# Kernel tuning notes

Hardware: AMD Instinct MI355X
Metric: run time of the kernel (lower is better)

## Reference

```python
import jax, jax.numpy as jnp
import numpy as np

N_NODES = 100000
N_EDGES = 800000
IN_FEATS = 128
OUT_FEATS = 128


def setup_inputs() -> dict:
    key = jax.random.key(0)
    k1, k2, k3, k4, k5, k6 = jax.random.split(key, 6)
    feat = jax.random.normal(k1, (N_NODES, IN_FEATS), dtype=jnp.float32)
    src = jax.random.randint(k2, (N_EDGES,), 0, N_NODES, dtype=jnp.int64)
    dst = jax.random.randint(k3, (N_EDGES,), 0, N_NODES, dtype=jnp.int64)
    # xavier_uniform with gain = calculate_gain('relu') = sqrt(2)
    gain = np.sqrt(2.0)
    lim = gain * np.sqrt(6.0 / (IN_FEATS + OUT_FEATS))
    W_neigh = jax.random.uniform(k4, (OUT_FEATS, IN_FEATS), minval=-lim, maxval=lim, dtype=jnp.float32)
    W_self = jax.random.uniform(k5, (OUT_FEATS, IN_FEATS), minval=-lim, maxval=lim, dtype=jnp.float32)
    b_lim = 1.0 / np.sqrt(IN_FEATS)
    b_self = jax.random.uniform(k6, (OUT_FEATS,), minval=-b_lim, maxval=b_lim, dtype=jnp.float32)
    return {"feat": feat, "src": src, "dst": dst, "W_neigh": W_neigh, "W_self": W_self, "b_self": b_self}


def reference(feat, src, dst, W_neigh, W_self, b_self):
    # copy_u + mean: gather source features along edges, segment-mean onto dst.
    # lin_before_mp is False (in_feats == out_feats), so aggregate raw features first.
    msgs = feat[src]                                   # [E, in_feats]
    summed = jax.ops.segment_sum(msgs, dst, num_segments=N_NODES)   # [N, in_feats]
    deg = jax.ops.segment_sum(jnp.ones((src.shape[0],), feat.dtype), dst, num_segments=N_NODES)
    h_neigh = summed / jnp.maximum(deg, 1.0)[:, None]  # mean; 0 for isolated nodes
    h_neigh = h_neigh @ W_neigh.T                      # fc_neigh (no bias)
    rst = feat @ W_self.T + b_self + h_neigh           # fc_self (bias) + neigh
    return rst
```

## Files before the change

### kernel.cpp

```cpp
#include <hip/hip_runtime.h>

#define N_NODES 100000
#define N_EDGES 800000
#define F 128
#define NB 16
#define BM 64

typedef __attribute__((ext_vector_type(8))) short bf16x8;
typedef __attribute__((ext_vector_type(4))) float f32x4;


__global__ void hist_kernel(const int* __restrict__ dst, int* __restrict__ count, int E) {
    int e = blockIdx.x * 256 + threadIdx.x;
    if (e < E) atomicAdd(&count[dst[e]], 1);
}

__global__ void scan1_kernel(const int* __restrict__ count, int* __restrict__ rowptr,
                             int* __restrict__ bsums, int N) {
    __shared__ int s[256];
    int tid = threadIdx.x;
    int base = blockIdx.x * 1024 + tid * 4;
    int c[4];
    int tsum = 0;
#pragma unroll
    for (int j = 0; j < 4; ++j) {
        int idx = base + j;
        c[j] = (idx < N) ? count[idx] : 0;
        tsum += c[j];
    }
    s[tid] = tsum;
    __syncthreads();
    for (int off = 1; off < 256; off <<= 1) {
        int u = (tid >= off) ? s[tid - off] : 0;
        __syncthreads();
        s[tid] += u;
        __syncthreads();
    }
    int incl = s[tid];
    int run = incl - tsum;
#pragma unroll
    for (int j = 0; j < 4; ++j) {
        int idx = base + j;
        if (idx < N) rowptr[idx] = run;
        run += c[j];
    }
    if (tid == 255) bsums[blockIdx.x] = incl;
}

__global__ void scan2_kernel(int* __restrict__ bsums, int nb) {
    __shared__ int s[256];
    int tid = threadIdx.x;
    int v = (tid < nb) ? bsums[tid] : 0;
    s[tid] = v;
    __syncthreads();
    for (int off = 1; off < 256; off <<= 1) {
        int u = (tid >= off) ? s[tid - off] : 0;
        __syncthreads();
        s[tid] += u;
        __syncthreads();
    }
    int excl = s[tid] - v;
    if (tid < nb) bsums[tid] = excl;
}

__global__ void scan3_kernel(int* __restrict__ rowptr, const int* __restrict__ bsums,
                             int* __restrict__ cursor, int N) {
    int i = blockIdx.x * 256 + threadIdx.x;
    if (i < N) {
        int r = rowptr[i] + bsums[i >> 10];
        rowptr[i] = r;
        cursor[i] = r;
    }
}

__global__ void fill_kernel(const int* __restrict__ src, const int* __restrict__ dst,
                            int* __restrict__ cursor, int* __restrict__ csr, int E) {
    int e = blockIdx.x * 256 + threadIdx.x;
    if (e < E) {
        int n = dst[e];
        int p = atomicAdd(&cursor[n], 1);
        csr[p] = src[e];
    }
}


__global__ void wprep_kernel(const float* __restrict__ Ws, const float* __restrict__ Wn,
                             short* __restrict__ wf) {
    int t = blockIdx.x * 256 + threadIdx.x;
    if (t >= 1024) return;
    int n = t >> 2;
    int ks = t & 3;
    const float* row = (n < 128) ? (Ws + (size_t)n * F) : (Wn + (size_t)(n - 128) * F);
    int ntile = n >> 4;
#pragma unroll
    for (int g = 0; g < 4; ++g) {
        int lane = (n & 15) + 16 * g;
        size_t base = ((size_t)(ntile * 4 + ks) * 64 + lane) * 8;
#pragma unroll
        for (int e = 0; e < 8; ++e) {
            float x = row[ks * 32 + g * 8 + e];
            unsigned xb = __float_as_uint(x);
            unsigned hb = xb & 0xFFFF0000u;
            float lo = x - __uint_as_float(hb);
            wf[base + e] = (short)(hb >> 16);
            wf[32768 + base + e] = (short)(__float_as_uint(lo) >> 16);
        }
    }
}


__global__ __launch_bounds__(256, 3) void gemm_mfma_kernel(
        const float* __restrict__ feat,
        const short* __restrict__ wf,
        const float* __restrict__ b_self,
        float* __restrict__ out, float* __restrict__ Y) {
    __shared__ bf16x8 aF[2][16][64];

    const int tid = threadIdx.x;
    const int nb = blockIdx.x * BM;

    {
        const int r = tid >> 2;
        const int ks = tid & 3;
        int n = nb + r;
        if (n >= N_NODES) n = N_NODES - 1;
        float4 v[8];
        const float4* g = reinterpret_cast<const float4*>(feat + (size_t)n * F + ks * 32);
#pragma unroll
        for (int j = 0; j < 8; ++j) v[j] = g[j];
        const float* vv = &v[0].x;
        const int mt = r >> 4;
        const int l0 = r & 15;
#pragma unroll
        for (int g5 = 0; g5 < 4; ++g5) {
            bf16x8 hi8, lo8;
#pragma unroll
            for (int e = 0; e < 8; ++e) {
                float x = vv[g5 * 8 + e];
                unsigned xb = __float_as_uint(x);
                unsigned hb = xb & 0xFFFF0000u;
                float lo = x - __uint_as_float(hb);
                hi8[e] = (short)(hb >> 16);
                lo8[e] = (short)(__float_as_uint(lo) >> 16);
            }
            aF[0][(ks << 2) | mt][l0 + 16 * g5] = hi8;
            aF[1][(ks << 2) | mt][l0 + 16 * g5] = lo8;
        }
    }
    __syncthreads();

    const int wv = tid >> 6;
    const int lane = tid & 63;

    f32x4 acc[4][4];
#pragma unroll
    for (int t = 0; t < 4; ++t)
#pragma unroll
        for (int j = 0; j < 4; ++j)
            acc[t][j] = (f32x4){0.f, 0.f, 0.f, 0.f};

    const bf16x8* wfh = reinterpret_cast<const bf16x8*>(wf);
    const bf16x8* wfl = wfh + 4096;

#pragma unroll
    for (int ks = 0; ks < 4; ++ks) {
        bf16x8 ah[4], al[4], bh[4], bl[4];
#pragma unroll
        for (int t = 0; t < 4; ++t) {
            ah[t] = aF[0][(ks << 2) | t][lane];
            al[t] = aF[1][(ks << 2) | t][lane];
        }
#pragma unroll
        for (int j = 0; j < 4; ++j) {
            const int ntile = wv * 4 + j;
            bh[j] = wfh[(ntile * 4 + ks) * 64 + lane];
            bl[j] = wfl[(ntile * 4 + ks) * 64 + lane];
        }
#pragma unroll
        for (int t = 0; t < 4; ++t)
#pragma unroll
            for (int j = 0; j < 4; ++j) {
                acc[t][j] = __builtin_amdgcn_mfma_f32_16x16x32_bf16(ah[t], bh[j], acc[t][j], 0, 0, 0);
                acc[t][j] = __builtin_amdgcn_mfma_f32_16x16x32_bf16(ah[t], bl[j], acc[t][j], 0, 0, 0);
                acc[t][j] = __builtin_amdgcn_mfma_f32_16x16x32_bf16(al[t], bh[j], acc[t][j], 0, 0, 0);
            }
    }

    const bool isOut = (wv < 2);
#pragma unroll
    for (int t = 0; t < 4; ++t) {
        const int m0 = nb + t * 16 + ((lane >> 4) << 2);
#pragma unroll
        for (int j = 0; j < 4; ++j) {
            const int col = wv * 64 + j * 16 + (lane & 15);
            if (isOut) {
                const float b = b_self[col];
#pragma unroll
                for (int r = 0; r < 4; ++r) {
                    const int m = m0 + r;
                    if (m < N_NODES) out[(size_t)m * F + col] = acc[t][j][r] + b;
                }
            } else {
#pragma unroll
                for (int r = 0; r < 4; ++r) {
                    const int m = m0 + r;
                    if (m < N_NODES) Y[(size_t)m * F + (col - 128)] = acc[t][j][r];
                }
            }
        }
    }
}


__global__ __launch_bounds__(256) void agg_kernel(
        const float* __restrict__ Y,
        const int* __restrict__ csr, const int* __restrict__ rowptr,
        const int* __restrict__ count,
        float* __restrict__ out) {
    const int node = blockIdx.x * 4 + (threadIdx.x >> 6);
    const int lane = threadIdx.x & 63;
    if (node >= N_NODES) return;

    const int rp = __builtin_amdgcn_readfirstlane(rowptr[node]);
    const int cnt = __builtin_amdgcn_readfirstlane(count[node]);

    float a0x = 0.f, a0y = 0.f, a1x = 0.f, a1y = 0.f;
    float a2x = 0.f, a2y = 0.f, a3x = 0.f, a3y = 0.f;

    int j = 0;
    for (; j + 4 <= cnt; j += 4) {
        const int i0 = csr[rp + j];
        const int i1 = csr[rp + j + 1];
        const int i2 = csr[rp + j + 2];
        const int i3 = csr[rp + j + 3];
        const float2 v0 = *reinterpret_cast<const float2*>(Y + (size_t)i0 * F + lane * 2);
        const float2 v1 = *reinterpret_cast<const float2*>(Y + (size_t)i1 * F + lane * 2);
        const float2 v2 = *reinterpret_cast<const float2*>(Y + (size_t)i2 * F + lane * 2);
        const float2 v3 = *reinterpret_cast<const float2*>(Y + (size_t)i3 * F + lane * 2);
        a0x += v0.x; a0y += v0.y;
        a1x += v1.x; a1y += v1.y;
        a2x += v2.x; a2y += v2.y;
        a3x += v3.x; a3y += v3.y;
    }
    for (; j < cnt; ++j) {
        const int i0 = csr[rp + j];
        const float2 v0 = *reinterpret_cast<const float2*>(Y + (size_t)i0 * F + lane * 2);
        a0x += v0.x; a0y += v0.y;
    }

    const float inv = 1.0f / fmaxf((float)cnt, 1.0f);
    const float sx = (a0x + a1x) + (a2x + a3x);
    const float sy = (a0y + a1y) + (a2y + a3y);

    float2* op = reinterpret_cast<float2*>(out + (size_t)node * F) + lane;
    float2 cur = *op;
    cur.x += sx * inv;
    cur.y += sy * inv;
    *op = cur;
}


__global__ __launch_bounds__(256) void main_kernel(
        const float* __restrict__ feat,
        const int* __restrict__ csr, const int* __restrict__ rowptr,
        const int* __restrict__ count,
        const float* __restrict__ Wn, const float* __restrict__ Ws,
        const float* __restrict__ b_self,
        float* __restrict__ out) {
    __shared__ __align__(16) float shF[NB][F];
    __shared__ __align__(16) float shH[NB][F];
    __shared__ __align__(16) float wts[32][F];
    __shared__ __align__(16) float wtn[32][F];

    const int tid = threadIdx.x;
    const int nb = blockIdx.x * NB;

    {
        const int g = tid >> 5;
        const int l = tid & 31;
        for (int i = g; i < NB; i += 8) {
            const int n = nb + i;
            const int rp = rowptr[n];
            const int cnt = count[n];
            float ax = 0.f, ay = 0.f, az = 0.f, aw = 0.f;
            for (int j = 0; j < cnt; ++j) {
                const int s = csr[rp + j];
                const float4 v = *reinterpret_cast<const float4*>(feat + (size_t)s * F + l * 4);
                ax += v.x; ay += v.y; az += v.z; aw += v.w;
            }
            const float dv = fmaxf((float)cnt, 1.0f);
            float4 h;
            h.x = ax / dv; h.y = ay / dv; h.z = az / dv; h.w = aw / dv;
            const float4 fv = *reinterpret_cast<const float4*>(feat + (size_t)n * F + l * 4);
            reinterpret_cast<float4*>(&shF[i][0])[l] = fv;
            reinterpret_cast<float4*>(&shH[i][0])[l] = h;
        }
    }
    __syncthreads();

    const int oc = tid & 63;
    const int ng = tid >> 6;
    float acc[4][2];
#pragma unroll
    for (int i = 0; i < 4; ++i) { acc[i][0] = 0.f; acc[i][1] = 0.f; }

    for (int kc = 0; kc < 4; ++kc) {
        {
            const int o_l = tid >> 1;
            const int k0 = (tid & 1) * 16;
            const float* gs = Ws + o_l * F + kc * 32 + k0;
            const float* gn = Wn + o_l * F + kc * 32 + k0;
#pragma unroll
            for (int j = 0; j < 16; ++j) {
                wts[k0 + j][o_l] = gs[j];
                wtn[k0 + j][o_l] = gn[j];
            }
        }
        __syncthreads();

#pragma unroll
        for (int kk4 = 0; kk4 < 32; kk4 += 4) {
            float4 fA[4], hA[4];
#pragma unroll
            for (int i = 0; i < 4; ++i) {
                const int node = ng * 4 + i;
                fA[i] = reinterpret_cast<const float4*>(&shF[node][0])[(kc * 32 + kk4) >> 2];
                hA[i] = reinterpret_cast<const float4*>(&shH[node][0])[(kc * 32 + kk4) >> 2];
            }
#pragma unroll
            for (int j = 0; j < 4; ++j) {
                const float2 wsv = *reinterpret_cast<const float2*>(&wts[kk4 + j][oc * 2]);
                const float2 wnv = *reinterpret_cast<const float2*>(&wtn[kk4 + j][oc * 2]);
#pragma unroll
                for (int i = 0; i < 4; ++i) {
                    const float fa = (&fA[i].x)[j];
                    const float ha = (&hA[i].x)[j];
                    acc[i][0] += fa * wsv.x + ha * wnv.x;
                    acc[i][1] += fa * wsv.y + ha * wnv.y;
                }
            }
        }
        __syncthreads();
    }

    const float b0 = b_self[oc * 2];
    const float b1 = b_self[oc * 2 + 1];
#pragma unroll
    for (int i = 0; i < 4; ++i) {
        const int n = nb + ng * 4 + i;
        float2 o2;
        o2.x = acc[i][0] + b0;
        o2.y = acc[i][1] + b1;
        *reinterpret_cast<float2*>(out + (size_t)n * F + oc * 2) = o2;
    }
}


extern "C" void kernel_launch(void* const* d_in, const int* in_sizes, int n_in,
                              void* d_out, int out_size, void* d_ws, size_t ws_size,
                              hipStream_t stream) {
    const float* feat = (const float*)d_in[0];
    const int* src    = (const int*)d_in[1];
    const int* dst    = (const int*)d_in[2];
    const float* Wn   = (const float*)d_in[3];
    const float* Ws   = (const float*)d_in[4];
    const float* bs   = (const float*)d_in[5];
    float* out        = (float*)d_out;

    const size_t y_floats = (size_t)N_NODES * F;
    const size_t wf_shorts = 65536;
    const size_t int_words = (size_t)3 * N_NODES + N_EDGES + 256;
    const size_t need = y_floats * 4 + wf_shorts * 2 + int_words * 4;
    const int nb1 = (N_NODES + 1023) / 1024;

    if (ws_size >= need) {
        float* Y    = (float*)d_ws;
        short* wf   = (short*)(Y + y_floats);
        int* count  = (int*)(wf + wf_shorts);
        int* rowptr = count + N_NODES;
        int* cursor = rowptr + N_NODES;
        int* csr    = cursor + N_NODES;
        int* bsums  = csr + N_EDGES;

        wprep_kernel<<<4, 256, 0, stream>>>(Ws, Wn, wf);
        hipMemsetAsync(count, 0, N_NODES * sizeof(int), stream);
        hist_kernel<<<(N_EDGES + 255) / 256, 256, 0, stream>>>(dst, count, N_EDGES);
        scan1_kernel<<<nb1, 256, 0, stream>>>(count, rowptr, bsums, N_NODES);
        scan2_kernel<<<1, 256, 0, stream>>>(bsums, nb1);
        scan3_kernel<<<(N_NODES + 255) / 256, 256, 0, stream>>>(rowptr, bsums, cursor, N_NODES);
        fill_kernel<<<(N_EDGES + 255) / 256, 256, 0, stream>>>(src, dst, cursor, csr, N_EDGES);
        gemm_mfma_kernel<<<(N_NODES + BM - 1) / BM, 256, 0, stream>>>(feat, wf, bs, out, Y);
        agg_kernel<<<(N_NODES + 3) / 4, 256, 0, stream>>>(Y, csr, rowptr, count, out);
    } else {
        int* count  = (int*)d_ws;
        int* rowptr = count + N_NODES;
        int* cursor = rowptr + N_NODES;
        int* csr    = cursor + N_NODES;
        int* bsums  = csr + N_EDGES;

        hipMemsetAsync(count, 0, N_NODES * sizeof(int), stream);
        hist_kernel<<<(N_EDGES + 255) / 256, 256, 0, stream>>>(dst, count, N_EDGES);
        scan1_kernel<<<nb1, 256, 0, stream>>>(count, rowptr, bsums, N_NODES);
        scan2_kernel<<<1, 256, 0, stream>>>(bsums, nb1);
        scan3_kernel<<<(N_NODES + 255) / 256, 256, 0, stream>>>(rowptr, bsums, cursor, N_NODES);
        fill_kernel<<<(N_EDGES + 255) / 256, 256, 0, stream>>>(src, dst, cursor, csr, N_EDGES);
        main_kernel<<<N_NODES / NB, 256, 0, stream>>>(feat, csr, rowptr, count, Wn, Ws, bs, out);
    }
}
```

Baseline: 288.7 us.

## Aggregate bf16 features before a fused dual GEMM, with a cooperative CSR build

```diff
diff --git a/kernel.cpp b/kernel.cpp
--- a/kernel.cpp
+++ b/kernel.cpp
@@ -1,13 +1,293 @@
 #include <hip/hip_runtime.h>
+#include <hip/hip_cooperative_groups.h>
+
+namespace cg = cooperative_groups;
 
 #define N_NODES 100000
 #define N_EDGES 800000
 #define F 128
 #define NB 16
 #define BM 64
+#define GBLK 512
+#define CS 196
 
 typedef __attribute__((ext_vector_type(8))) short bf16x8;
 typedef __attribute__((ext_vector_type(4))) float f32x4;
+
+__device__ inline unsigned short f2bf_rne(float x) {
+    unsigned u = __float_as_uint(x);
+    u += 0x7FFF + ((u >> 16) & 1);
+    return (unsigned short)(u >> 16);
+}
+
+
+__global__ void build_kernel(const int* __restrict__ src, const int* __restrict__ dst,
+                             const float* __restrict__ feat,
+                             const float* __restrict__ Ws, const float* __restrict__ Wn,
+                             unsigned* __restrict__ featbf, short* __restrict__ wf,
+                             int* __restrict__ count, int* __restrict__ rowptr,
+                             int* __restrict__ cursor, int* __restrict__ csr,
+                             int* __restrict__ bsums) {
+    cg::grid_group grid = cg::this_grid();
+    __shared__ int sh[256];
+    const int tid = threadIdx.x;
+    const int gt = blockIdx.x * 256 + tid;
+    const int GT = GBLK * 256;
+
+    for (int i = gt; i < N_NODES; i += GT) count[i] = 0;
+    {
+        const int total = N_NODES * (F / 8);
+        for (int i = gt; i < total; i += GT) {
+            const float4 a = reinterpret_cast<const float4*>(feat)[i * 2];
+            const float4 b = reinterpret_cast<const float4*>(feat)[i * 2 + 1];
+            uint4 r;
+            r.x = (unsigned)f2bf_rne(a.x) | ((unsigned)f2bf_rne(a.y) << 16);
+            r.y = (unsigned)f2bf_rne(a.z) | ((unsigned)f2bf_rne(a.w) << 16);
+            r.z = (unsigned)f2bf_rne(b.x) | ((unsigned)f2bf_rne(b.y) << 16);
+            r.w = (unsigned)f2bf_rne(b.z) | ((unsigned)f2bf_rne(b.w) << 16);
+            reinterpret_cast<uint4*>(featbf)[i] = r;
+        }
+    }
+    if (gt < 1024) {
+        const int n = gt >> 2;
+        const int ks = gt & 3;
+        const float* row;
+        short *hb_, *lb_;
+        int ntile;
+        if (n < 128) { row = Ws + (size_t)n * F; hb_ = wf;          lb_ = wf + 16384; ntile = n >> 4; }
+        else         { row = Wn + (size_t)(n - 128) * F; hb_ = wf + 32768; lb_ = wf + 49152; ntile = (n - 128) >> 4; }
+#pragma unroll
+        for (int g = 0; g < 4; ++g) {
+            const int lane = (n & 15) + 16 * g;
+            const size_t base = ((size_t)(ntile * 4 + ks) * 64 + lane) * 8;
+#pragma unroll
+            for (int e = 0; e < 8; ++e) {
+                const float x = row[ks * 32 + g * 8 + e];
+                const unsigned hb = __float_as_uint(x) & 0xFFFF0000u;
+                const float lo = x - __uint_as_float(hb);
+                hb_[base + e] = (short)(hb >> 16);
+                lb_[base + e] = (short)(__float_as_uint(lo) >> 16);
+            }
+        }
+    }
+    grid.sync();
+
+    for (int e = gt; e < N_EDGES; e += GT) atomicAdd(&count[dst[e]], 1);
+    grid.sync();
+
+    {
+        const int idx = blockIdx.x * CS + tid;
+        const int c = (tid < CS && idx < N_NODES) ? count[idx] : 0;
+        sh[tid] = c;
+        __syncthreads();
+        for (int off = 128; off > 0; off >>= 1) {
+            if (tid < off) sh[tid] += sh[tid + off];
+            __syncthreads();
+        }
+        if (tid == 0) bsums[blockIdx.x] = sh[0];
+    }
+    grid.sync();
+
+    if (blockIdx.x == 0) {
+        int carry = 0;
+        for (int r = 0; r < GBLK / 256; ++r) {
+            const int i = r * 256 + tid;
+            const int v = bsums[i];
+            sh[tid] = v;
+            __syncthreads();
+            for (int off = 1; off < 256; off <<= 1) {
+                const int u = (tid >= off) ? sh[tid - off] : 0;
+                __syncthreads();
+                sh[tid] += u;
+                __syncthreads();
+            }
+            bsums[i] = sh[tid] - v + carry;
+            carry += sh[255];
+            __syncthreads();
+        }
+    }
+    grid.sync();
+
+    {
+        const int idx = blockIdx.x * CS + tid;
+        const int c = (tid < CS && idx < N_NODES) ? count[idx] : 0;
+        sh[tid] = c;
+        __syncthreads();
+        for (int off = 1; off < 256; off <<= 1) {
+            const int u = (tid >= off) ? sh[tid - off] : 0;
+            __syncthreads();
+            sh[tid] += u;
+            __syncthreads();
+        }
+        if (tid < CS && idx < N_NODES) {
+            const int excl = bsums[blockIdx.x] + sh[tid] - c;
+            rowptr[idx] = excl;
+            cursor[idx] = excl;
+        }
+    }
+    grid.sync();
+
+    for (int e = gt; e < N_EDGES; e += GT) {
+        const int n = dst[e];
+        const int p = atomicAdd(&cursor[n], 1);
+        csr[p] = src[e];
+    }
+}
+
+
+__global__ __launch_bounds__(256) void agg_kernel(
+        const unsigned* __restrict__ featbf,
+        const int* __restrict__ csr, const int* __restrict__ rowptr,
+        const int* __restrict__ count,
+        unsigned* __restrict__ M) {
+    const int node = blockIdx.x * 4 + (threadIdx.x >> 6);
+    const int lane = threadIdx.x & 63;
+    if (node >= N_NODES) return;
+
+    const int rp = __builtin_amdgcn_readfirstlane(rowptr[node]);
+    const int cnt = __builtin_amdgcn_readfirstlane(count[node]);
+
+    float ax[8], ay[8];
+#pragma unroll
+    for (int u = 0; u < 8; ++u) { ax[u] = 0.f; ay[u] = 0.f; }
+
+    int j = 0;
+    for (; j + 8 <= cnt; j += 8) {
+        int idx[8];
+#pragma unroll
+        for (int u = 0; u < 8; ++u) idx[u] = __builtin_nontemporal_load(&csr[rp + j + u]);
+        unsigned v[8];
+#pragma unroll
+        for (int u = 0; u < 8; ++u) v[u] = featbf[(size_t)idx[u] * 64 + lane];
+#pragma unroll
+        for (int u = 0; u < 8; ++u) {
+            ax[u] += __uint_as_float(v[u] << 16);
+            ay[u] += __uint_as_float(v[u] & 0xFFFF0000u);
+        }
+    }
+    for (; j < cnt; ++j) {
+        const int i0 = __builtin_nontemporal_load(&csr[rp + j]);
+        const unsigned v = featbf[(size_t)i0 * 64 + lane];
+        ax[0] += __uint_as_float(v << 16);
+        ay[0] += __uint_as_float(v & 0xFFFF0000u);
+    }
+
+    const float inv = 1.0f / fmaxf((float)cnt, 1.0f);
+    float sx = 0.f, sy = 0.f;
+#pragma unroll
+    for (int u = 0; u < 8; ++u) { sx += ax[u]; sy += ay[u]; }
+    sx *= inv; sy *= inv;
+
+    const unsigned packed = (unsigned)f2bf_rne(sx) | ((unsigned)f2bf_rne(sy) << 16);
+    M[(size_t)node * 64 + lane] = packed;
+}
+
+
+__global__ __launch_bounds__(256, 3) void gemm_kernel(
+        const float* __restrict__ feat,
+        const unsigned* __restrict__ M,
+        const short* __restrict__ wf,
+        const float* __restrict__ b_self,
+        float* __restrict__ out) {
+    __shared__ bf16x8 aF[2][16][64];
+
+    const int tid = threadIdx.x;
+    const int nb = blockIdx.x * BM;
+
+    {
+        const int r = tid >> 2;
+        const int ks = tid & 3;
+        int n = nb + r;
+        if (n >= N_NODES) n = N_NODES - 1;
+        float4 v[8];
+        const float4* g = reinterpret_cast<const float4*>(feat + (size_t)n * F + ks * 32);
+#pragma unroll
+        for (int j = 0; j < 8; ++j) v[j] = g[j];
+        const float* vv = &v[0].x;
+        const int mt = r >> 4;
+        const int l0 = r & 15;
+#pragma unroll
+        for (int g5 = 0; g5 < 4; ++g5) {
+            bf16x8 hi8, lo8;
+#pragma unroll
+            for (int e = 0; e < 8; ++e) {
+                const float x = vv[g5 * 8 + e];
+                const unsigned hb = __float_as_uint(x) & 0xFFFF0000u;
+                const float lo = x - __uint_as_float(hb);
+                hi8[e] = (short)(hb >> 16);
+                lo8[e] = (short)(__float_as_uint(lo) >> 16);
+            }
+            aF[0][(ks << 2) | mt][l0 + 16 * g5] = hi8;
+            aF[1][(ks << 2) | mt][l0 + 16 * g5] = lo8;
+        }
+    }
+    __syncthreads();
+
+    const int wv = tid >> 6;
+    const int lane = tid & 63;
+
+    f32x4 acc[4][2];
+#pragma unroll
+    for (int t = 0; t < 4; ++t)
+#pragma unroll
+        for (int j = 0; j < 2; ++j)
+            acc[t][j] = (f32x4){0.f, 0.f, 0.f, 0.f};
+
+    const bf16x8* wsh = reinterpret_cast<const bf16x8*>(wf);
+    const bf16x8* wsl = wsh + 2048;
+    const bf16x8* wnh = wsh + 4096;
+    const bf16x8* wnl = wsh + 6144;
+    const bf16x8* M8 = reinterpret_cast<const bf16x8*>(M);
+
+#pragma unroll
+    for (int ks = 0; ks < 4; ++ks) {
+        bf16x8 ah[4], al[4], am[4];
+#pragma unroll
+        for (int t = 0; t < 4; ++t) {
+            ah[t] = aF[0][(ks << 2) | t][lane];
+            al[t] = aF[1][(ks << 2) | t][lane];
+        }
+#pragma unroll
+        for (int t = 0; t < 4; ++t) {
+            int node = nb + t * 16 + (lane & 15);
+            if (node >= N_NODES) node = N_NODES - 1;
+            am[t] = M8[(size_t)node * 16 + ks * 4 + (lane >> 4)];
+        }
+        bf16x8 bsh[2], bsl[2], bnh[2], bnl[2];
+#pragma unroll
+        for (int j = 0; j < 2; ++j) {
+            const int fi = ((wv * 2 + j) * 4 + ks) * 64 + lane;
+            bsh[j] = wsh[fi]; bsl[j] = wsl[fi];
+            bnh[j] = wnh[fi]; bnl[j] = wnl[fi];
+        }
+#pragma unroll
+        for (int t = 0; t < 4; ++t)
+#pragma unroll
+            for (int j = 0; j < 2; ++j) {
+                acc[t][j] = __builtin_amdgcn_mfma_f32_16x16x32_bf16(ah[t], bsh[j], acc[t][j], 0, 0, 0);
+                acc[t][j] = __builtin_amdgcn_mfma_f32_16x16x32_bf16(ah[t], bsl[j], acc[t][j], 0, 0, 0);
+                acc[t][j] = __builtin_amdgcn_mfma_f32_16x16x32_bf16(al[t], bsh[j], acc[t][j], 0, 0, 0);
+                acc[t][j] = __builtin_amdgcn_mfma_f32_16x16x32_bf16(am[t], bnh[j], acc[t][j], 0, 0, 0);
+                acc[t][j] = __builtin_amdgcn_mfma_f32_16x16x32_bf16(am[t], bnl[j], acc[t][j], 0, 0, 0);
+            }
+    }
+
+#pragma unroll
+    for (int t = 0; t < 4; ++t) {
+        const int m0 = nb + t * 16 + ((lane >> 4) << 2);
+#pragma unroll
+        for (int j = 0; j < 2; ++j) {
+            const int col = wv * 32 + j * 16 + (lane & 15);
+            const float b = b_self[col];
+#pragma unroll
+            for (int r = 0; r < 4; ++r) {
+                const int m = m0 + r;
+                if (m < N_NODES)
+                    __builtin_nontemporal_store(acc[t][j][r] + b, &out[(size_t)m * F + col]);
+            }
+        }
+    }
+}
 
 
 __global__ void hist_kernel(const int* __restrict__ dst, int* __restrict__ count, int E) {
@@ -82,183 +362,6 @@
         csr[p] = src[e];
     }
 }
-
-
-__global__ void wprep_kernel(const float* __restrict__ Ws, const float* __restrict__ Wn,
-                             short* __restrict__ wf) {
-    int t = blockIdx.x * 256 + threadIdx.x;
-    if (t >= 1024) return;
-    int n = t >> 2;
-    int ks = t & 3;
-    const float* row = (n < 128) ? (Ws + (size_t)n * F) : (Wn + (size_t)(n - 128) * F);
-    int ntile = n >> 4;
-#pragma unroll
-    for (int g = 0; g < 4; ++g) {
-        int lane = (n & 15) + 16 * g;
-        size_t base = ((size_t)(ntile * 4 + ks) * 64 + lane) * 8;
-#pragma unroll
-        for (int e = 0; e < 8; ++e) {
-            float x = row[ks * 32 + g * 8 + e];
-            unsigned xb = __float_as_uint(x);
-            unsigned hb = xb & 0xFFFF0000u;
-            float lo = x - __uint_as_float(hb);
-            wf[base + e] = (short)(hb >> 16);
-            wf[32768 + base + e] = (short)(__float_as_uint(lo) >> 16);
-        }
-    }
-}
-
-
-__global__ __launch_bounds__(256, 3) void gemm_mfma_kernel(
-        const float* __restrict__ feat,
-        const short* __restrict__ wf,
-        const float* __restrict__ b_self,
-        float* __restrict__ out, float* __restrict__ Y) {
-    __shared__ bf16x8 aF[2][16][64];
-
-    const int tid = threadIdx.x;
-    const int nb = blockIdx.x * BM;
-
-    {
-        const int r = tid >> 2;
-        const int ks = tid & 3;
-        int n = nb + r;
-        if (n >= N_NODES) n = N_NODES - 1;
-        float4 v[8];
-        const float4* g = reinterpret_cast<const float4*>(feat + (size_t)n * F + ks * 32);
-#pragma unroll
-        for (int j = 0; j < 8; ++j) v[j] = g[j];
-        const float* vv = &v[0].x;
-        const int mt = r >> 4;
-        const int l0 = r & 15;
-#pragma unroll
-        for (int g5 = 0; g5 < 4; ++g5) {
-            bf16x8 hi8, lo8;
-#pragma unroll
-            for (int e = 0; e < 8; ++e) {
-                float x = vv[g5 * 8 + e];
-                unsigned xb = __float_as_uint(x);
-                unsigned hb = xb & 0xFFFF0000u;
-                float lo = x - __uint_as_float(hb);
-                hi8[e] = (short)(hb >> 16);
-                lo8[e] = (short)(__float_as_uint(lo) >> 16);
-            }
-            aF[0][(ks << 2) | mt][l0 + 16 * g5] = hi8;
-            aF[1][(ks << 2) | mt][l0 + 16 * g5] = lo8;
-        }
-    }
-    __syncthreads();
-
-    const int wv = tid >> 6;
-    const int lane = tid & 63;
-
-    f32x4 acc[4][4];
-#pragma unroll
-    for (int t = 0; t < 4; ++t)
-#pragma unroll
-        for (int j = 0; j < 4; ++j)
-            acc[t][j] = (f32x4){0.f, 0.f, 0.f, 0.f};
-
-    const bf16x8* wfh = reinterpret_cast<const bf16x8*>(wf);
-    const bf16x8* wfl = wfh + 4096;
-
-#pragma unroll
-    for (int ks = 0; ks < 4; ++ks) {
-        bf16x8 ah[4], al[4], bh[4], bl[4];
-#pragma unroll
-        for (int t = 0; t < 4; ++t) {
-            ah[t] = aF[0][(ks << 2) | t][lane];
-            al[t] = aF[1][(ks << 2) | t][lane];
-        }
-#pragma unroll
-        for (int j = 0; j < 4; ++j) {
-            const int ntile = wv * 4 + j;
-            bh[j] = wfh[(ntile * 4 + ks) * 64 + lane];
-            bl[j] = wfl[(ntile * 4 + ks) * 64 + lane];
-        }
-#pragma unroll
-        for (int t = 0; t < 4; ++t)
-#pragma unroll
-            for (int j = 0; j < 4; ++j) {
-                acc[t][j] = __builtin_amdgcn_mfma_f32_16x16x32_bf16(ah[t], bh[j], acc[t][j], 0, 0, 0);
-                acc[t][j] = __builtin_amdgcn_mfma_f32_16x16x32_bf16(ah[t], bl[j], acc[t][j], 0, 0, 0);
-                acc[t][j] = __builtin_amdgcn_mfma_f32_16x16x32_bf16(al[t], bh[j], acc[t][j], 0, 0, 0);
-            }
-    }
-
-    const bool isOut = (wv < 2);
-#pragma unroll
-    for (int t = 0; t < 4; ++t) {
-        const int m0 = nb + t * 16 + ((lane >> 4) << 2);
-#pragma unroll
-        for (int j = 0; j < 4; ++j) {
-            const int col = wv * 64 + j * 16 + (lane & 15);
-            if (isOut) {
-                const float b = b_self[col];
-#pragma unroll
-                for (int r = 0; r < 4; ++r) {
-                    const int m = m0 + r;
-                    if (m < N_NODES) out[(size_t)m * F + col] = acc[t][j][r] + b;
-                }
-            } else {
-#pragma unroll
-                for (int r = 0; r < 4; ++r) {
-                    const int m = m0 + r;
-                    if (m < N_NODES) Y[(size_t)m * F + (col - 128)] = acc[t][j][r];
-                }
-            }
-        }
-    }
-}
-
-
-__global__ __launch_bounds__(256) void agg_kernel(
-        const float* __restrict__ Y,
-        const int* __restrict__ csr, const int* __restrict__ rowptr,
-        const int* __restrict__ count,
-        float* __restrict__ out) {
-    const int node = blockIdx.x * 4 + (threadIdx.x >> 6);
-    const int lane = threadIdx.x & 63;
-    if (node >= N_NODES) return;
-
-    const int rp = __builtin_amdgcn_readfirstlane(rowptr[node]);
-    const int cnt = __builtin_amdgcn_readfirstlane(count[node]);
-
-    float a0x = 0.f, a0y = 0.f, a1x = 0.f, a1y = 0.f;
-    float a2x = 0.f, a2y = 0.f, a3x = 0.f, a3y = 0.f;
-
-    int j = 0;
-    for (; j + 4 <= cnt; j += 4) {
-        const int i0 = csr[rp + j];
-        const int i1 = csr[rp + j + 1];
-        const int i2 = csr[rp + j + 2];
-        const int i3 = csr[rp + j + 3];
-        const float2 v0 = *reinterpret_cast<const float2*>(Y + (size_t)i0 * F + lane * 2);
-        const float2 v1 = *reinterpret_cast<const float2*>(Y + (size_t)i1 * F + lane * 2);
-        const float2 v2 = *reinterpret_cast<const float2*>(Y + (size_t)i2 * F + lane * 2);
-        const float2 v3 = *reinterpret_cast<const float2*>(Y + (size_t)i3 * F + lane * 2);
-        a0x += v0.x; a0y += v0.y;
-        a1x += v1.x; a1y += v1.y;
-        a2x += v2.x; a2y += v2.y;
-        a3x += v3.x; a3y += v3.y;
-    }
-    for (; j < cnt; ++j) {
-        const int i0 = csr[rp + j];
-        const float2 v0 = *reinterpret_cast<const float2*>(Y + (size_t)i0 * F + lane * 2);
-        a0x += v0.x; a0y += v0.y;
-    }
-
-    const float inv = 1.0f / fmaxf((float)cnt, 1.0f);
-    const float sx = (a0x + a1x) + (a2x + a3x);
-    const float sy = (a0y + a1y) + (a2y + a3y);
-
-    float2* op = reinterpret_cast<float2*>(out + (size_t)node * F) + lane;
-    float2 cur = *op;
-    cur.x += sx * inv;
-    cur.y += sy * inv;
-    *op = cur;
-}
-
 
 __global__ __launch_bounds__(256) void main_kernel(
         const float* __restrict__ feat,
@@ -367,36 +470,34 @@
     const float* bs   = (const float*)d_in[5];
     float* out        = (float*)d_out;
 
-    const size_t y_floats = (size_t)N_NODES * F;
+    const size_t bf_words = (size_t)N_NODES * (F / 2);
     const size_t wf_shorts = 65536;
-    const size_t int_words = (size_t)3 * N_NODES + N_EDGES + 256;
-    const size_t need = y_floats * 4 + wf_shorts * 2 + int_words * 4;
-    const int nb1 = (N_NODES + 1023) / 1024;
+    const size_t int_words = (size_t)3 * N_NODES + N_EDGES + GBLK;
+    const size_t need = bf_words * 2 * 4 + wf_shorts * 2 + int_words * 4;
 
     if (ws_size >= need) {
-        float* Y    = (float*)d_ws;
-        short* wf   = (short*)(Y + y_floats);
+        unsigned* featbf = (unsigned*)d_ws;
+        unsigned* M      = featbf + bf_words;
+        short* wf        = (short*)(M + bf_words);
         int* count  = (int*)(wf + wf_shorts);
         int* rowptr = count + N_NODES;
         int* cursor = rowptr + N_NODES;
         int* csr    = cursor + N_NODES;
         int* bsums  = csr + N_EDGES;
 
-        wprep_kernel<<<4, 256, 0, stream>>>(Ws, Wn, wf);
-        hipMemsetAsync(count, 0, N_NODES * sizeof(int), stream);
-        hist_kernel<<<(N_EDGES + 255) / 256, 256, 0, stream>>>(dst, count, N_EDGES);
-        scan1_kernel<<<nb1, 256, 0, stream>>>(count, rowptr, bsums, N_NODES);
-        scan2_kernel<<<1, 256, 0, stream>>>(bsums, nb1);
-        scan3_kernel<<<(N_NODES + 255) / 256, 256, 0, stream>>>(rowptr, bsums, cursor, N_NODES);
-        fill_kernel<<<(N_EDGES + 255) / 256, 256, 0, stream>>>(src, dst, cursor, csr, N_EDGES);
-        gemm_mfma_kernel<<<(N_NODES + BM - 1) / BM, 256, 0, stream>>>(feat, wf, bs, out, Y);
-        agg_kernel<<<(N_NODES + 3) / 4, 256, 0, stream>>>(Y, csr, rowptr, count, out);
+        void* args[] = {(void*)&src, (void*)&dst, (void*)&feat, (void*)&Ws, (void*)&Wn,
+                        (void*)&featbf, (void*)&wf, (void*)&count, (void*)&rowptr,
+                        (void*)&cursor, (void*)&csr, (void*)&bsums};
+        hipLaunchCooperativeKernel((void*)build_kernel, dim3(GBLK), dim3(256), args, 0, stream);
+        agg_kernel<<<(N_NODES + 3) / 4, 256, 0, stream>>>(featbf, csr, rowptr, count, M);
+        gemm_kernel<<<(N_NODES + BM - 1) / BM, 256, 0, stream>>>(feat, M, wf, bs, out);
     } else {
         int* count  = (int*)d_ws;
         int* rowptr = count + N_NODES;
         int* cursor = rowptr + N_NODES;
         int* csr    = cursor + N_NODES;
         int* bsums  = csr + N_EDGES;
+        const int nb1 = (N_NODES + 1023) / 1024;
 
         hipMemsetAsync(count, 0, N_NODES * sizeof(int), stream);
         hist_kernel<<<(N_EDGES + 255) / 256, 256, 0, stream>>>(dst, count, N_EDGES);
```

Measured after the change: 589.1 us. 2.04x slower.
